# Kernel optimization log

Measured on AMD Instinct MI355X. Metric: run time of the kernel, lower is better.

## Reference

```python
import jax, jax.numpy as jnp
import numpy as np

N, G, E = 100000, 32768, 1000000
F, H = 64, 64


def _mlp(x, w1, b1, w2, b2):
    # Linear -> SiLU -> Linear (matches nn.Sequential in the torch module)
    return jax.nn.silu(x @ w1 + b1) @ w2 + b2


def setup_inputs() -> dict:
    key = jax.random.key(0)
    ks = jax.random.split(key, 24)

    def lin(k, fan_in, fan_out):
        s = 1.0 / np.sqrt(fan_in)
        kw, kb = jax.random.split(k)
        w = jax.random.uniform(kw, (fan_in, fan_out), jnp.float32, -s, s)
        b = jax.random.uniform(kb, (fan_out,), jnp.float32, -s, s)
        return w, b

    node_w1, node_b1 = lin(ks[0], F, H)
    node_w2, node_b2 = lin(ks[1], H, H)
    edge_w1, edge_b1 = lin(ks[2], 6, H)
    edge_w2, edge_b2 = lin(ks[3], H, H)
    msg_w1, msg_b1 = lin(ks[4], 2 * H, H)
    msg_w2, msg_b2 = lin(ks[5], H, H)
    upd_w1, upd_b1 = lin(ks[6], H, H)
    upd_w2, upd_b2 = lin(ks[7], H, H)

    return {
        "node_features": jax.random.normal(ks[8], (N, F), jnp.float32),
        "node_pos": jax.random.normal(ks[9], (N, 3), jnp.float32),
        "grid_pos": jax.random.normal(ks[10], (G, 3), jnp.float32),
        "orientations": jax.random.normal(ks[11], (N, 3, 3), jnp.float32),
        "edge_index": jnp.stack([
            jax.random.randint(ks[12], (E,), 0, N),
            jax.random.randint(ks[13], (E,), 0, G),
        ]),
        "node_w1": node_w1, "node_b1": node_b1, "node_w2": node_w2, "node_b2": node_b2,
        "edge_w1": edge_w1, "edge_b1": edge_b1, "edge_w2": edge_w2, "edge_b2": edge_b2,
        "msg_w1": msg_w1, "msg_b1": msg_b1, "msg_w2": msg_w2, "msg_b2": msg_b2,
        "upd_w1": upd_w1, "upd_b1": upd_b1, "upd_w2": upd_w2, "upd_b2": upd_b2,
    }


def reference(node_features, node_pos, grid_pos, orientations, edge_index,
              node_w1, node_b1, node_w2, node_b2,
              edge_w1, edge_b1, edge_w2, edge_b2,
              msg_w1, msg_b1, msg_w2, msg_b2,
              upd_w1, upd_b1, upd_w2, upd_b2):
    source, target = edge_index[0], edge_index[1]
    num_grid = grid_pos.shape[0]

    # node MLP
    h_node = _mlp(node_features, node_w1, node_b1, node_w2, node_b2)  # [N,H]

    # per-edge message with orientation-aware projection
    pos_s = node_pos[source]                 # [E,3]
    rel = grid_pos[target] - pos_s           # [E,3]
    # bmm(rel[:,None,:], R[source]).squeeze(1) == einsum ei,eij->ej
    trel = jnp.einsum("ei,eij->ej", rel, orientations[source])
    edge_attr = jnp.concatenate([pos_s, trel], axis=-1)        # [E,6]
    e_feat = _mlp(edge_attr, edge_w1, edge_b1, edge_w2, edge_b2)
    msg_in = jnp.concatenate([h_node[source], e_feat], axis=-1)  # [E,2H]
    messages = _mlp(msg_in, msg_w1, msg_b1, msg_w2, msg_b2)      # [E,H]

    # scatter-mean into grid buckets (mask out-of-range targets)
    valid = (target >= 0) & (target < num_grid)
    idx = jnp.where(valid, target, 0)
    msg_masked = jnp.where(valid[:, None], messages, 0.0)
    sums = jax.ops.segment_sum(msg_masked, idx, num_segments=num_grid)
    cnts = jax.ops.segment_sum(valid.astype(jnp.float32), idx, num_segments=num_grid)
    grid_feat = sums / jnp.maximum(cnts, 1.0)[:, None]

    return _mlp(grid_feat, upd_w1, upd_b1, upd_w2, upd_b2)  # [G,H]
```

## Files before the change

kernel.cpp:

```cpp
#include <hip/hip_runtime.h>
#include <hip/hip_bf16.h>
#include <cstdint>

typedef __attribute__((ext_vector_type(8))) short short8;
typedef __attribute__((ext_vector_type(4))) float f32x4;
typedef unsigned short u16;

__device__ __forceinline__ float b2f(u16 u) {
  union { unsigned int i; float f; } v; v.i = ((unsigned int)u) << 16; return v.f;
}
__device__ __forceinline__ u16 f2b(float f) {
  __hip_bfloat16 h = __float2bfloat16(f);
  union { __hip_bfloat16 h; u16 u; } v; v.h = h; return v.u;
}
__device__ __forceinline__ float silu_f(float x) { return x / (1.0f + __expf(-x)); }

__device__ __forceinline__ float loadF(const void* p, long i, int isf32) {
  if (isf32) return ((const float*)p)[i];
  return b2f(((const u16*)p)[i]);
}

__device__ __forceinline__ int sniffbit(u16 u) {
  unsigned e = (u >> 7) & 0xffu;
  return (e >= 0xC0u || (e < 0x40u && (u & 0x7fffu) != 0)) ? 1 : 0;
}
__device__ __forceinline__ int detect1(const void* p, int n) {
  const u16* q = (const u16*)p;
  int m = n < 512 ? n : 512;
  int h = 0;
  for (int k = 0; k < m; ++k) h += sniffbit(q[k]);
  return h >= 2;
}

struct Ptrs { const void* p[20]; };

#define FW_EW1 0
#define FW_UW1 384
#define FW_UW2 4480
#define FW_UB1 8576
#define FW_UB2 8640
#define FW_EB1 8704
#define FW_EB2 8768
#define FW_MB1 8832
#define FW_MB2 8896
#define FW_TOTAL 8960

#define IMG_EW2 0
#define IMG_MW1 4608
#define IMG_MW2 13312
#define IMG_TOTAL 17920

#define PREP_BLOCKS 105
#define HIST_BLOCKS 1024

__global__ __launch_bounds__(256) void fused_a(
    Ptrs a, u16* __restrict__ img, float* __restrict__ fw,
    const int* __restrict__ eidx, int* __restrict__ cnt,
    const void* x, u16* __restrict__ hout, int nrows,
    long E, int G, int nodeBlocks)
{
  const int t = threadIdx.x;
  const int b = blockIdx.x;

  if (b >= nodeBlocks + PREP_BLOCKS) {
    long i = (long)(b - nodeBlocks - PREP_BLOCKS) * 256 + t;
    const long stride = (long)HIST_BLOCKS * 256;
    for (; i < E; i += stride) {
      int tg = eidx[E + i];
      if (tg >= 0 && tg < G) atomicAdd(&cnt[tg], 1);
    }
    return;
  }

  if (b >= nodeBlocks) {
    int i = (b - nodeBlocks) * 256 + t;
    if (i < IMG_TOTAL) {
      const void* bp; int n; long si; bool real;
      if (i < IMG_MW1) { int nn = i / 72, k = i % 72; bp = a.p[10]; n = 4096; real = k < 64; si = (long)k * 64 + nn; }
      else if (i < IMG_MW2) { int t2 = i - IMG_MW1; int nn = t2 / 136, k = t2 % 136; bp = a.p[12]; n = 8192; real = k < 128; si = (long)k * 64 + nn; }
      else { int t2 = i - IMG_MW2; int nn = t2 / 72, k = t2 % 72; bp = a.p[14]; n = 4096; real = k < 64; si = (long)k * 64 + nn; }
      u16 val = 0;
      if (real) { int isf = detect1(bp, n); val = f2b(loadF(bp, si, isf)); }
      img[i] = val;
    } else if (i < IMG_TOTAL + FW_TOTAL) {
      int j = i - IMG_TOTAL;
      const void* bp; int n; long si;
      if (j < 384)        { bp = a.p[8];  n = 384;  si = j; }
      else if (j < 4480)  { bp = a.p[16]; n = 4096; si = j - 384; }
      else if (j < 8576)  { bp = a.p[18]; n = 4096; si = j - 4480; }
      else {
        int bb = j - 8576; int seg = bb >> 6; si = bb & 63; n = 64;
        switch (seg) {
          case 0: bp = a.p[17]; break;
          case 1: bp = a.p[19]; break;
          case 2: bp = a.p[9];  break;
          case 3: bp = a.p[11]; break;
          case 4: bp = a.p[13]; break;
          default: bp = a.p[15]; break;
        }
      }
      int isf = detect1(bp, n);
      fw[j] = loadF(bp, si, isf);
    }
    return;
  }

  __shared__ float xs[64][68];
  __shared__ float w1s[64][68];
  __shared__ float w2s[64][68];
  __shared__ float b1s[64];
  __shared__ float b2s[64];
  __shared__ int nd[5];
  if (t < 5) nd[t] = 0;
  __syncthreads();
  {
    int c = 0;
    const u16* q0 = (const u16*)x;
    for (int i = t; i < 2048; i += 256) c += sniffbit(q0[i]);
    if (c) atomicAdd(&nd[0], c);
    c = 0;
    const u16* q1 = (const u16*)a.p[4];
    for (int i = t; i < 2048; i += 256) c += sniffbit(q1[i]);
    if (c) atomicAdd(&nd[1], c);
    c = 0;
    const u16* q2 = (const u16*)a.p[6];
    for (int i = t; i < 2048; i += 256) c += sniffbit(q2[i]);
    if (c) atomicAdd(&nd[2], c);
    if (t < 64) {
      if (sniffbit(((const u16*)a.p[5])[t])) atomicAdd(&nd[3], 1);
      if (sniffbit(((const u16*)a.p[7])[t])) atomicAdd(&nd[4], 1);
    }
  }
  __syncthreads();
  const int xf = nd[0] >= 2, f1 = nd[1] >= 2, f2 = nd[2] >= 2;
  const int fb1 = nd[3] >= 2, fb2 = nd[4] >= 2;
  const long rbase = (long)b * 64;
  for (int i = t; i < 4096; i += 256) {
    int k = i >> 6, cc = i & 63;
    w1s[k][cc] = loadF(a.p[4], i, f1);
    w2s[k][cc] = loadF(a.p[6], i, f2);
  }
  if (t < 64) { b1s[t] = loadF(a.p[5], t, fb1); b2s[t] = loadF(a.p[7], t, fb2); }
  {
    int row = t >> 2, ch = t & 3;
    long rg = rbase + row;
    if (rg < nrows) {
      if (xf) {
        const float* xp = (const float*)x + rg * 64 + ch * 16;
#pragma unroll
        for (int m = 0; m < 16; ++m) xs[row][ch * 16 + m] = xp[m];
      } else {
        const u16* xp = (const u16*)x + rg * 64 + ch * 16;
#pragma unroll
        for (int m = 0; m < 16; ++m) xs[row][ch * 16 + m] = b2f(xp[m]);
      }
    } else {
#pragma unroll
      for (int m = 0; m < 16; ++m) xs[row][ch * 16 + m] = 0.f;
    }
  }
  __syncthreads();
  const int r0 = (t >> 4) * 4, c0 = (t & 15) * 4;
  float acc[4][4];
#pragma unroll
  for (int i = 0; i < 4; ++i)
#pragma unroll
    for (int j = 0; j < 4; ++j) acc[i][j] = b1s[c0 + j];
  for (int k = 0; k < 64; ++k) {
    float w0 = w1s[k][c0], w1v = w1s[k][c0 + 1], w2v = w1s[k][c0 + 2], w3v = w1s[k][c0 + 3];
#pragma unroll
    for (int i = 0; i < 4; ++i) {
      float av = xs[r0 + i][k];
      acc[i][0] = fmaf(av, w0, acc[i][0]);
      acc[i][1] = fmaf(av, w1v, acc[i][1]);
      acc[i][2] = fmaf(av, w2v, acc[i][2]);
      acc[i][3] = fmaf(av, w3v, acc[i][3]);
    }
  }
  __syncthreads();
#pragma unroll
  for (int i = 0; i < 4; ++i)
#pragma unroll
    for (int j = 0; j < 4; ++j) xs[r0 + i][c0 + j] = silu_f(acc[i][j]);
  __syncthreads();
  float acc2[4][4];
#pragma unroll
  for (int i = 0; i < 4; ++i)
#pragma unroll
    for (int j = 0; j < 4; ++j) acc2[i][j] = b2s[c0 + j];
  for (int k = 0; k < 64; ++k) {
    float w0 = w2s[k][c0], w1v = w2s[k][c0 + 1], w2v = w2s[k][c0 + 2], w3v = w2s[k][c0 + 3];
#pragma unroll
    for (int i = 0; i < 4; ++i) {
      float av = xs[r0 + i][k];
      acc2[i][0] = fmaf(av, w0, acc2[i][0]);
      acc2[i][1] = fmaf(av, w1v, acc2[i][1]);
      acc2[i][2] = fmaf(av, w2v, acc2[i][2]);
      acc2[i][3] = fmaf(av, w3v, acc2[i][3]);
    }
  }
#pragma unroll
  for (int i = 0; i < 4; ++i) {
    long rg = rbase + r0 + i;
    if (rg < nrows) {
#pragma unroll
      for (int j = 0; j < 4; ++j) hout[rg * 64 + c0 + j] = f2b(acc2[i][j]);
    }
  }
}

__global__ __launch_bounds__(256) void scan_k(const int* __restrict__ cnt,
                                              int* __restrict__ cursor,
                                              int* __restrict__ bsum, int G) {
  __shared__ int sd[256];
  const int t = threadIdx.x;
  int i = blockIdx.x * 256 + t;
  int v = (i < G) ? cnt[i] : 0;
  sd[t] = v;
  __syncthreads();
  for (int off = 1; off < 256; off <<= 1) {
    int x2 = (t >= off) ? sd[t - off] : 0;
    __syncthreads();
    sd[t] += x2;
    __syncthreads();
  }
  if (i < G) cursor[i] = sd[t] - v;
  if (t == 255) bsum[blockIdx.x] = sd[255];
}

__global__ __launch_bounds__(256) void scat_k(const int* __restrict__ eidx,
                                              int* __restrict__ cursor,
                                              const int* __restrict__ bsum,
                                              unsigned int* __restrict__ pkS,
                                              int* __restrict__ evp,
                                              long E, int G, int NB2) {
  __shared__ int bo[256];
  const int t = threadIdx.x;
  int v = (t < NB2) ? bsum[t] : 0;
  bo[t] = v;
  __syncthreads();
  for (int off = 1; off < 256; off <<= 1) {
    int x2 = (t >= off) ? bo[t - off] : 0;
    __syncthreads();
    bo[t] += x2;
    __syncthreads();
  }
  if (blockIdx.x == 0 && t == 0) *evp = bo[NB2 - 1];
  int excl = bo[t] - v;
  __syncthreads();
  bo[t] = excl;
  __syncthreads();
  long i = (long)blockIdx.x * 256 + t;
  const long stride = (long)gridDim.x * 256;
  for (; i < E; i += stride) {
    int tg = eidx[E + i];
    if (tg >= 0 && tg < G) {
      int s = eidx[i];
      int p = atomicAdd(&cursor[tg], 1) + bo[tg >> 8];
      pkS[p] = (unsigned int)s | ((unsigned int)tg << 17);
    }
  }
}

#define ETILES 4

__global__ __launch_bounds__(256, 5) void edge_kernel(
    const void* node_pos, const void* grid_pos, const void* orient,
    const unsigned int* __restrict__ pkS, const int* __restrict__ evp,
    const u16* __restrict__ h_node, const u16* __restrict__ img,
    const float* __restrict__ fw,
    float* __restrict__ sums, int G)
{
  __shared__ __align__(16) u16 hA[64][136];
  __shared__ __align__(16) u16 ef1[64][72];
  __shared__ float eaf[64][6];
  __shared__ float w1e[6][64];
  __shared__ float biasE[4][64];
  __shared__ int src_s[64];
  __shared__ int tgt_s[64];
  __shared__ int det[3];
  float (*msgf)[66] = (float (*)[66])&hA[0][0];

  const int t = threadIdx.x;
  if (t < 3) det[t] = 0;
  __syncthreads();
  {
    int grp = t >> 6;
    if (grp < 3) {
      const u16* qq = (const u16*)(grp == 0 ? node_pos : grp == 1 ? grid_pos : orient);
      int cth = 0, l = t & 63;
      for (int i = l; i < 2048; i += 64) cth += sniffbit(qq[i]);
      if (cth) atomicAdd(&det[grp], cth);
    }
  }
  for (int i = t; i < 384; i += 256) w1e[i / 64][i % 64] = fw[FW_EW1 + i];
  { int seg = t >> 6, cc = t & 63; biasE[seg][cc] = fw[FW_EB1 + seg * 64 + cc]; }
  __syncthreads();
  const int pf = det[0] >= 2, gf = det[1] >= 2, of = det[2] >= 2;
  const int Ev = *evp;

  const int lane = t & 63, w = t >> 6;
  const int q = lane >> 4, c = lane & 15;
  const int m0 = w * 16;
  const u16* wE2 = img + IMG_EW2;
  const u16* wM1 = img + IMG_MW1;
  const u16* wM2 = img + IMG_MW2;
  const f32x4 z = {0.f, 0.f, 0.f, 0.f};

  for (int tile = 0; tile < ETILES; ++tile) {
    long base = ((long)blockIdx.x * ETILES + tile) * 64;
    if (base >= Ev) break;
    __syncthreads();
    if (t < 64) {
      long eg = base + t;
      int s, tg;
      if (eg < Ev) {
        unsigned int pk = pkS[eg];
        s = (int)(pk & 0x1FFFFu);
        tg = (int)(pk >> 17);
      } else { s = 0; tg = -1; }
      src_s[t] = s;
      tgt_s[t] = tg;
      int tgc = (tg >= 0) ? tg : 0;
      float ps[3], rel[3], tr[3];
#pragma unroll
      for (int i = 0; i < 3; ++i) {
        ps[i] = loadF(node_pos, (long)s * 3 + i, pf);
        rel[i] = loadF(grid_pos, (long)tgc * 3 + i, gf) - ps[i];
      }
#pragma unroll
      for (int j = 0; j < 3; ++j) tr[j] = 0.f;
#pragma unroll
      for (int i = 0; i < 3; ++i)
#pragma unroll
        for (int j = 0; j < 3; ++j)
          tr[j] = fmaf(rel[i], loadF(orient, (long)s * 9 + i * 3 + j, of), tr[j]);
      eaf[t][0] = ps[0]; eaf[t][1] = ps[1]; eaf[t][2] = ps[2];
      eaf[t][3] = tr[0]; eaf[t][4] = tr[1]; eaf[t][5] = tr[2];
    }
    __syncthreads();
    {
      int e = t >> 2, ch = t & 3;
      const u16* hp = h_node + (long)src_s[e] * 64 + ch * 16;
      short8 v0 = *(const short8*)hp;
      short8 v1 = *(const short8*)(hp + 8);
      *(short8*)&hA[e][ch * 16] = v0;
      *(short8*)&hA[e][ch * 16 + 8] = v1;
    }
    __syncthreads();

    {
      int e = t >> 2, c0 = (t & 3) * 16;
      float a0 = eaf[e][0], a1 = eaf[e][1], a2 = eaf[e][2];
      float a3 = eaf[e][3], a4 = eaf[e][4], a5 = eaf[e][5];
      __align__(16) u16 tmp[16];
#pragma unroll
      for (int j = 0; j < 16; ++j) {
        int cc = c0 + j;
        float acc = biasE[0][cc];
        acc = fmaf(a0, w1e[0][cc], acc);
        acc = fmaf(a1, w1e[1][cc], acc);
        acc = fmaf(a2, w1e[2][cc], acc);
        acc = fmaf(a3, w1e[3][cc], acc);
        acc = fmaf(a4, w1e[4][cc], acc);
        acc = fmaf(a5, w1e[5][cc], acc);
        tmp[j] = f2b(silu_f(acc));
      }
      *(short8*)&ef1[e][c0] = *(const short8*)tmp;
      *(short8*)&ef1[e][c0 + 8] = *(const short8*)(tmp + 8);
    }
    __syncthreads();
    {
      short8 a0 = *(const short8*)&ef1[m0 + c][q * 8];
      short8 a1 = *(const short8*)&ef1[m0 + c][32 + q * 8];
#pragma unroll
      for (int nt = 0; nt < 4; ++nt) {
        short8 b0 = *(const short8*)&wE2[(nt * 16 + c) * 72 + q * 8];
        short8 b1v = *(const short8*)&wE2[(nt * 16 + c) * 72 + 32 + q * 8];
        f32x4 acc = __builtin_amdgcn_mfma_f32_16x16x32_bf16(a0, b0, z, 0, 0, 0);
        acc = __builtin_amdgcn_mfma_f32_16x16x32_bf16(a1, b1v, acc, 0, 0, 0);
#pragma unroll
        for (int r = 0; r < 4; ++r) {
          int row = m0 + q * 4 + r, col = nt * 16 + c;
          hA[row][64 + col] = f2b(acc[r] + biasE[1][col]);
        }
      }
    }
    __syncthreads();
    {
      short8 a0 = *(const short8*)&hA[m0 + c][q * 8];
      short8 a1 = *(const short8*)&hA[m0 + c][32 + q * 8];
      short8 a2 = *(const short8*)&hA[m0 + c][64 + q * 8];
      short8 a3 = *(const short8*)&hA[m0 + c][96 + q * 8];
#pragma unroll
      for (int nt = 0; nt < 4; ++nt) {
        const u16* wp = &wM1[(nt * 16 + c) * 136];
        f32x4 acc = __builtin_amdgcn_mfma_f32_16x16x32_bf16(a0, *(const short8*)(wp + q * 8), z, 0, 0, 0);
        acc = __builtin_amdgcn_mfma_f32_16x16x32_bf16(a1, *(const short8*)(wp + 32 + q * 8), acc, 0, 0, 0);
        acc = __builtin_amdgcn_mfma_f32_16x16x32_bf16(a2, *(const short8*)(wp + 64 + q * 8), acc, 0, 0, 0);
        acc = __builtin_amdgcn_mfma_f32_16x16x32_bf16(a3, *(const short8*)(wp + 96 + q * 8), acc, 0, 0, 0);
#pragma unroll
        for (int r = 0; r < 4; ++r) {
          int row = m0 + q * 4 + r, col = nt * 16 + c;
          ef1[row][col] = f2b(silu_f(acc[r] + biasE[2][col]));
        }
      }
    }
    __syncthreads();
    {
      short8 a0 = *(const short8*)&ef1[m0 + c][q * 8];
      short8 a1 = *(const short8*)&ef1[m0 + c][32 + q * 8];
#pragma unroll
      for (int nt = 0; nt < 4; ++nt) {
        short8 b0 = *(const short8*)&wM2[(nt * 16 + c) * 72 + q * 8];
        short8 b1v = *(const short8*)&wM2[(nt * 16 + c) * 72 + 32 + q * 8];
        f32x4 acc = __builtin_amdgcn_mfma_f32_16x16x32_bf16(a0, b0, z, 0, 0, 0);
        acc = __builtin_amdgcn_mfma_f32_16x16x32_bf16(a1, b1v, acc, 0, 0, 0);
#pragma unroll
        for (int r = 0; r < 4; ++r) {
          int row = m0 + q * 4 + r, col = nt * 16 + c;
          msgf[row][col] = acc[r] + biasE[3][col];
        }
      }
    }
    __syncthreads();
    {
      int col = lane;
      int r0 = w * 16;
      int cur = tgt_s[r0];
      float run = msgf[r0][col];
      bool lopen = (r0 == 0) ? true : (tgt_s[r0 - 1] == cur);
#pragma unroll
      for (int r2 = 1; r2 < 16; ++r2) {
        int r = r0 + r2;
        int tg = tgt_s[r];
        float v = msgf[r][col];
        if (tg == cur) {
          run += v;
        } else {
          if (cur >= 0) {
            if (lopen) unsafeAtomicAdd(&sums[(long)cur * 64 + col], run);
            else sums[(long)cur * 64 + col] = run;
          }
          cur = tg; run = v; lopen = false;
        }
      }
      bool ropen = (r0 + 16 >= 64) ? true : (tgt_s[r0 + 16] == cur);
      if (cur >= 0) {
        if (lopen || ropen) unsafeAtomicAdd(&sums[(long)cur * 64 + col], run);
        else sums[(long)cur * 64 + col] = run;
      }
    }
  }
}

__global__ __launch_bounds__(256) void upd_mlp(
    const float* __restrict__ sums, const int* __restrict__ cnt,
    const float* __restrict__ fw, float* __restrict__ out, int nrows)
{
  __shared__ float xs[64][68];
  __shared__ float w1s[64][68];
  __shared__ float w2s[64][68];
  __shared__ float b1s[64];
  __shared__ float b2s[64];
  const int t = threadIdx.x;
  const long rbase = (long)blockIdx.x * 64;
  for (int i = t; i < 4096; i += 256) {
    int k = i >> 6, cc = i & 63;
    w1s[k][cc] = fw[FW_UW1 + i];
    w2s[k][cc] = fw[FW_UW2 + i];
  }
  if (t < 64) { b1s[t] = fw[FW_UB1 + t]; b2s[t] = fw[FW_UB2 + t]; }
  {
    int row = t >> 2, ch = t & 3;
    long rg = rbase + row;
    if (rg < nrows) {
      float inv = 1.0f / fmaxf((float)cnt[rg], 1.0f);
      const float* p = sums + rg * 64 + ch * 16;
#pragma unroll
      for (int m = 0; m < 16; ++m) xs[row][ch * 16 + m] = p[m] * inv;
    } else {
#pragma unroll
      for (int m = 0; m < 16; ++m) xs[row][ch * 16 + m] = 0.f;
    }
  }
  __syncthreads();
  const int r0 = (t >> 4) * 4, c0 = (t & 15) * 4;
  float acc[4][4];
#pragma unroll
  for (int i = 0; i < 4; ++i)
#pragma unroll
    for (int j = 0; j < 4; ++j) acc[i][j] = b1s[c0 + j];
  for (int k = 0; k < 64; ++k) {
    float w0 = w1s[k][c0], w1v = w1s[k][c0 + 1], w2v = w1s[k][c0 + 2], w3v = w1s[k][c0 + 3];
#pragma unroll
    for (int i = 0; i < 4; ++i) {
      float av = xs[r0 + i][k];
      acc[i][0] = fmaf(av, w0, acc[i][0]);
      acc[i][1] = fmaf(av, w1v, acc[i][1]);
      acc[i][2] = fmaf(av, w2v, acc[i][2]);
      acc[i][3] = fmaf(av, w3v, acc[i][3]);
    }
  }
  __syncthreads();
#pragma unroll
  for (int i = 0; i < 4; ++i)
#pragma unroll
    for (int j = 0; j < 4; ++j) xs[r0 + i][c0 + j] = silu_f(acc[i][j]);
  __syncthreads();
  float acc2[4][4];
#pragma unroll
  for (int i = 0; i < 4; ++i)
#pragma unroll
    for (int j = 0; j < 4; ++j) acc2[i][j] = b2s[c0 + j];
  for (int k = 0; k < 64; ++k) {
    float w0 = w2s[k][c0], w1v = w2s[k][c0 + 1], w2v = w2s[k][c0 + 2], w3v = w2s[k][c0 + 3];
#pragma unroll
    for (int i = 0; i < 4; ++i) {
      float av = xs[r0 + i][k];
      acc2[i][0] = fmaf(av, w0, acc2[i][0]);
      acc2[i][1] = fmaf(av, w1v, acc2[i][1]);
      acc2[i][2] = fmaf(av, w2v, acc2[i][2]);
      acc2[i][3] = fmaf(av, w3v, acc2[i][3]);
    }
  }
#pragma unroll
  for (int i = 0; i < 4; ++i) {
    long rg = rbase + r0 + i;
    if (rg < nrows) {
#pragma unroll
      for (int j = 0; j < 4; ++j) out[rg * 64 + c0 + j] = acc2[i][j];
    }
  }
}

extern "C" void kernel_launch(void* const* d_in, const int* in_sizes, int n_in,
                              void* d_out, int out_size, void* d_ws, size_t ws_size,
                              hipStream_t stream) {
  const int N = in_sizes[1] / 3;
  const int G = in_sizes[2] / 3;
  const long E = (long)in_sizes[4] / 2;
  const int NB2 = (G + 255) / 256;
  const int nodeBlocks = (N + 63) / 64;

  char* ws = (char*)d_ws;
  float* sums = (float*)ws;
  size_t off = (size_t)G * 256;
  int* cnt = (int*)(ws + off);     off += (size_t)G * 4;
  int* cursor = (int*)(ws + off);  off += (size_t)G * 4;
  int* bsum = (int*)(ws + off);    off += 1024;
  int* evp = (int*)(ws + off);     off += 256;
  unsigned int* pkS = (unsigned int*)(ws + off); off += (size_t)E * 4;
  u16* h_node = (u16*)(ws + off);  off += (size_t)N * 128;
  u16* img = (u16*)(ws + off);     off += (size_t)IMG_TOTAL * 2;
  float* fw = (float*)(ws + off);

  hipMemsetAsync(ws, 0, (size_t)G * 260, stream);

  Ptrs a;
  const int map[20] = {0,1,2,3, 5,6,7,8, 9,10,11,12, 13,14,15,16, 17,18,19,20};
  for (int i = 0; i < 20; ++i) a.p[i] = d_in[map[i]];

  fused_a<<<nodeBlocks + PREP_BLOCKS + HIST_BLOCKS, 256, 0, stream>>>(
      a, img, fw, (const int*)d_in[4], cnt, d_in[0], h_node, N, E, G, nodeBlocks);
  scan_k<<<NB2, 256, 0, stream>>>(cnt, cursor, bsum, G);
  scat_k<<<1024, 256, 0, stream>>>((const int*)d_in[4], cursor, bsum, pkS, evp, E, G, NB2);
  edge_kernel<<<(int)((E + ETILES * 64 - 1) / (ETILES * 64)), 256, 0, stream>>>(
      d_in[1], d_in[2], d_in[3], pkS, evp, h_node, img, fw, sums, G);
  upd_mlp<<<(G + 63) / 64, 256, 0, stream>>>(sums, cnt, fw, (float*)d_out, G);
}
```

Measured before the change: 488.0 us.

## Hoist dtype detection into a dedicated kernel and enlarge edge tiles per block

Adds a tiny detect_k kernel that computes a per-input fp32/bf16 flag once and stores it in workspace. fused_a and edge_kernel now read these flags instead of re-sniffing thousands of elements in every block, and detect1 no longer runs per element in the prep blocks. Other changes: edge tiles per block go from 4 to 8, the src shared array is replaced by re-reading pkS, a per-tile barrier moves, and the packed scatter store becomes nontemporal. The cost is one extra kernel launch and a dependency on the flags buffer.

After: 474.4 us. -2.8%, faster.

```diff
diff --git a/kernel.cpp b/kernel.cpp
--- a/kernel.cpp
+++ b/kernel.cpp
@@ -24,15 +24,8 @@
   unsigned e = (u >> 7) & 0xffu;
   return (e >= 0xC0u || (e < 0x40u && (u & 0x7fffu) != 0)) ? 1 : 0;
 }
-__device__ __forceinline__ int detect1(const void* p, int n) {
-  const u16* q = (const u16*)p;
-  int m = n < 512 ? n : 512;
-  int h = 0;
-  for (int k = 0; k < m; ++k) h += sniffbit(q[k]);
-  return h >= 2;
-}
-
-struct Ptrs { const void* p[20]; };
+
+struct Ptrs { const void* p[20]; int n[20]; };
 
 #define FW_EW1 0
 #define FW_UW1 384
@@ -53,17 +46,32 @@
 #define PREP_BLOCKS 105
 #define HIST_BLOCKS 1024
 
+__global__ __launch_bounds__(256) void detect_k(Ptrs a, int* flags) {
+  int j = blockIdx.x;
+  const u16* q = (const u16*)a.p[j];
+  int n = a.n[j];
+  int m = n < 4096 ? n : 4096;
+  int cnt = 0;
+  for (int i = threadIdx.x; i < m; i += 256) cnt += sniffbit(q[i]);
+  __shared__ int tot;
+  if (threadIdx.x == 0) tot = 0;
+  __syncthreads();
+  if (cnt) atomicAdd(&tot, cnt);
+  __syncthreads();
+  if (threadIdx.x == 0) flags[j] = (tot >= 2) ? 1 : 0;
+}
+
 __global__ __launch_bounds__(256) void fused_a(
-    Ptrs a, u16* __restrict__ img, float* __restrict__ fw,
+    Ptrs a, const int* __restrict__ flags,
+    u16* __restrict__ img, float* __restrict__ fw,
     const int* __restrict__ eidx, int* __restrict__ cnt,
-    const void* x, u16* __restrict__ hout, int nrows,
-    long E, int G, int nodeBlocks)
+    u16* __restrict__ hout, int nrows, long E, int G)
 {
   const int t = threadIdx.x;
   const int b = blockIdx.x;
 
-  if (b >= nodeBlocks + PREP_BLOCKS) {
-    long i = (long)(b - nodeBlocks - PREP_BLOCKS) * 256 + t;
+  if (b < HIST_BLOCKS) {
+    long i = (long)b * 256 + t;
     const long stride = (long)HIST_BLOCKS * 256;
     for (; i < E; i += stride) {
       int tg = eidx[E + i];
@@ -72,35 +80,34 @@
     return;
   }
 
-  if (b >= nodeBlocks) {
-    int i = (b - nodeBlocks) * 256 + t;
+  if (b < HIST_BLOCKS + PREP_BLOCKS) {
+    int i = (b - HIST_BLOCKS) * 256 + t;
     if (i < IMG_TOTAL) {
-      const void* bp; int n; long si; bool real;
-      if (i < IMG_MW1) { int nn = i / 72, k = i % 72; bp = a.p[10]; n = 4096; real = k < 64; si = (long)k * 64 + nn; }
-      else if (i < IMG_MW2) { int t2 = i - IMG_MW1; int nn = t2 / 136, k = t2 % 136; bp = a.p[12]; n = 8192; real = k < 128; si = (long)k * 64 + nn; }
-      else { int t2 = i - IMG_MW2; int nn = t2 / 72, k = t2 % 72; bp = a.p[14]; n = 4096; real = k < 64; si = (long)k * 64 + nn; }
+      const void* bp; int fl; long si; bool real;
+      if (i < IMG_MW1) { int nn = i / 72, k = i % 72; bp = a.p[10]; fl = flags[10]; real = k < 64; si = (long)k * 64 + nn; }
+      else if (i < IMG_MW2) { int t2 = i - IMG_MW1; int nn = t2 / 136, k = t2 % 136; bp = a.p[12]; fl = flags[12]; real = k < 128; si = (long)k * 64 + nn; }
+      else { int t2 = i - IMG_MW2; int nn = t2 / 72, k = t2 % 72; bp = a.p[14]; fl = flags[14]; real = k < 64; si = (long)k * 64 + nn; }
       u16 val = 0;
-      if (real) { int isf = detect1(bp, n); val = f2b(loadF(bp, si, isf)); }
+      if (real) val = f2b(loadF(bp, si, fl));
       img[i] = val;
     } else if (i < IMG_TOTAL + FW_TOTAL) {
       int j = i - IMG_TOTAL;
-      const void* bp; int n; long si;
-      if (j < 384)        { bp = a.p[8];  n = 384;  si = j; }
-      else if (j < 4480)  { bp = a.p[16]; n = 4096; si = j - 384; }
-      else if (j < 8576)  { bp = a.p[18]; n = 4096; si = j - 4480; }
+      const void* bp; int fl; long si;
+      if (j < 384)        { bp = a.p[8];  fl = flags[8];  si = j; }
+      else if (j < 4480)  { bp = a.p[16]; fl = flags[16]; si = j - 384; }
+      else if (j < 8576)  { bp = a.p[18]; fl = flags[18]; si = j - 4480; }
       else {
-        int bb = j - 8576; int seg = bb >> 6; si = bb & 63; n = 64;
+        int bb = j - 8576; int seg = bb >> 6; si = bb & 63;
         switch (seg) {
-          case 0: bp = a.p[17]; break;
-          case 1: bp = a.p[19]; break;
-          case 2: bp = a.p[9];  break;
-          case 3: bp = a.p[11]; break;
-          case 4: bp = a.p[13]; break;
-          default: bp = a.p[15]; break;
+          case 0: bp = a.p[17]; fl = flags[17]; break;
+          case 1: bp = a.p[19]; fl = flags[19]; break;
+          case 2: bp = a.p[9];  fl = flags[9];  break;
+          case 3: bp = a.p[11]; fl = flags[11]; break;
+          case 4: bp = a.p[13]; fl = flags[13]; break;
+          default: bp = a.p[15]; fl = flags[15]; break;
         }
       }
-      int isf = detect1(bp, n);
-      fw[j] = loadF(bp, si, isf);
+      fw[j] = loadF(bp, si, fl);
     }
     return;
   }
@@ -110,31 +117,9 @@
   __shared__ float w2s[64][68];
   __shared__ float b1s[64];
   __shared__ float b2s[64];
-  __shared__ int nd[5];
-  if (t < 5) nd[t] = 0;
-  __syncthreads();
-  {
-    int c = 0;
-    const u16* q0 = (const u16*)x;
-    for (int i = t; i < 2048; i += 256) c += sniffbit(q0[i]);
-    if (c) atomicAdd(&nd[0], c);
-    c = 0;
-    const u16* q1 = (const u16*)a.p[4];
-    for (int i = t; i < 2048; i += 256) c += sniffbit(q1[i]);
-    if (c) atomicAdd(&nd[1], c);
-    c = 0;
-    const u16* q2 = (const u16*)a.p[6];
-    for (int i = t; i < 2048; i += 256) c += sniffbit(q2[i]);
-    if (c) atomicAdd(&nd[2], c);
-    if (t < 64) {
-      if (sniffbit(((const u16*)a.p[5])[t])) atomicAdd(&nd[3], 1);
-      if (sniffbit(((const u16*)a.p[7])[t])) atomicAdd(&nd[4], 1);
-    }
-  }
-  __syncthreads();
-  const int xf = nd[0] >= 2, f1 = nd[1] >= 2, f2 = nd[2] >= 2;
-  const int fb1 = nd[3] >= 2, fb2 = nd[4] >= 2;
-  const long rbase = (long)b * 64;
+  const void* x = a.p[0];
+  const int xf = flags[0], f1 = flags[4], fb1 = flags[5], f2 = flags[6], fb2 = flags[7];
+  const long rbase = (long)(b - HIST_BLOCKS - PREP_BLOCKS) * 64;
   for (int i = t; i < 4096; i += 256) {
     int k = i >> 6, cc = i & 63;
     w1s[k][cc] = loadF(a.p[4], i, f1);
@@ -257,18 +242,18 @@
     if (tg >= 0 && tg < G) {
       int s = eidx[i];
       int p = atomicAdd(&cursor[tg], 1) + bo[tg >> 8];
-      pkS[p] = (unsigned int)s | ((unsigned int)tg << 17);
-    }
-  }
-}
-
-#define ETILES 4
+      __builtin_nontemporal_store((unsigned int)s | ((unsigned int)tg << 17), pkS + p);
+    }
+  }
+}
+
+#define ETILES 8
 
 __global__ __launch_bounds__(256, 5) void edge_kernel(
     const void* node_pos, const void* grid_pos, const void* orient,
     const unsigned int* __restrict__ pkS, const int* __restrict__ evp,
     const u16* __restrict__ h_node, const u16* __restrict__ img,
-    const float* __restrict__ fw,
+    const float* __restrict__ fw, const int* __restrict__ flags,
     float* __restrict__ sums, int G)
 {
   __shared__ __align__(16) u16 hA[64][136];
@@ -276,28 +261,15 @@
   __shared__ float eaf[64][6];
   __shared__ float w1e[6][64];
   __shared__ float biasE[4][64];
-  __shared__ int src_s[64];
   __shared__ int tgt_s[64];
-  __shared__ int det[3];
   float (*msgf)[66] = (float (*)[66])&hA[0][0];
 
   const int t = threadIdx.x;
-  if (t < 3) det[t] = 0;
-  __syncthreads();
-  {
-    int grp = t >> 6;
-    if (grp < 3) {
-      const u16* qq = (const u16*)(grp == 0 ? node_pos : grp == 1 ? grid_pos : orient);
-      int cth = 0, l = t & 63;
-      for (int i = l; i < 2048; i += 64) cth += sniffbit(qq[i]);
-      if (cth) atomicAdd(&det[grp], cth);
-    }
-  }
+  const int pf = flags[1], gf = flags[2], of = flags[3];
+  const int Ev = *evp;
   for (int i = t; i < 384; i += 256) w1e[i / 64][i % 64] = fw[FW_EW1 + i];
   { int seg = t >> 6, cc = t & 63; biasE[seg][cc] = fw[FW_EB1 + seg * 64 + cc]; }
   __syncthreads();
-  const int pf = det[0] >= 2, gf = det[1] >= 2, of = det[2] >= 2;
-  const int Ev = *evp;
 
   const int lane = t & 63, w = t >> 6;
   const int q = lane >> 4, c = lane & 15;
@@ -310,16 +282,14 @@
   for (int tile = 0; tile < ETILES; ++tile) {
     long base = ((long)blockIdx.x * ETILES + tile) * 64;
     if (base >= Ev) break;
-    __syncthreads();
     if (t < 64) {
       long eg = base + t;
-      int s, tg;
+      int s = 0, tg = -1;
       if (eg < Ev) {
         unsigned int pk = pkS[eg];
         s = (int)(pk & 0x1FFFFu);
         tg = (int)(pk >> 17);
-      } else { s = 0; tg = -1; }
-      src_s[t] = s;
+      }
       tgt_s[t] = tg;
       int tgc = (tg >= 0) ? tg : 0;
       float ps[3], rel[3], tr[3];
@@ -338,10 +308,12 @@
       eaf[t][0] = ps[0]; eaf[t][1] = ps[1]; eaf[t][2] = ps[2];
       eaf[t][3] = tr[0]; eaf[t][4] = tr[1]; eaf[t][5] = tr[2];
     }
-    __syncthreads();
     {
       int e = t >> 2, ch = t & 3;
-      const u16* hp = h_node + (long)src_s[e] * 64 + ch * 16;
+      long eg = base + e;
+      int s = 0;
+      if (eg < Ev) s = (int)(pkS[eg] & 0x1FFFFu);
+      const u16* hp = h_node + (long)s * 64 + ch * 16;
       short8 v0 = *(const short8*)hp;
       short8 v1 = *(const short8*)(hp + 8);
       *(short8*)&hA[e][ch * 16] = v0;
@@ -451,6 +423,7 @@
         else sums[(long)cur * 64 + col] = run;
       }
     }
+    __syncthreads();
   }
 }
 
@@ -550,6 +523,7 @@
   int* cursor = (int*)(ws + off);  off += (size_t)G * 4;
   int* bsum = (int*)(ws + off);    off += 1024;
   int* evp = (int*)(ws + off);     off += 256;
+  int* flags = (int*)(ws + off);   off += 256;
   unsigned int* pkS = (unsigned int*)(ws + off); off += (size_t)E * 4;
   u16* h_node = (u16*)(ws + off);  off += (size_t)N * 128;
   u16* img = (u16*)(ws + off);     off += (size_t)IMG_TOTAL * 2;
@@ -559,13 +533,14 @@
 
   Ptrs a;
   const int map[20] = {0,1,2,3, 5,6,7,8, 9,10,11,12, 13,14,15,16, 17,18,19,20};
-  for (int i = 0; i < 20; ++i) a.p[i] = d_in[map[i]];
-
-  fused_a<<<nodeBlocks + PREP_BLOCKS + HIST_BLOCKS, 256, 0, stream>>>(
-      a, img, fw, (const int*)d_in[4], cnt, d_in[0], h_node, N, E, G, nodeBlocks);
+  for (int i = 0; i < 20; ++i) { a.p[i] = d_in[map[i]]; a.n[i] = in_sizes[map[i]]; }
+
+  detect_k<<<20, 256, 0, stream>>>(a, flags);
+  fused_a<<<HIST_BLOCKS + PREP_BLOCKS + nodeBlocks, 256, 0, stream>>>(
+      a, flags, img, fw, (const int*)d_in[4], cnt, h_node, N, E, G);
   scan_k<<<NB2, 256, 0, stream>>>(cnt, cursor, bsum, G);
   scat_k<<<1024, 256, 0, stream>>>((const int*)d_in[4], cursor, bsum, pkS, evp, E, G, NB2);
   edge_kernel<<<(int)((E + ETILES * 64 - 1) / (ETILES * 64)), 256, 0, stream>>>(
-      d_in[1], d_in[2], d_in[3], pkS, evp, h_node, img, fw, sums, G);
+      d_in[1], d_in[2], d_in[3], pkS, evp, h_node, img, fw, flags, sums, G);
   upd_mlp<<<(G + 63) / 64, 256, 0, stream>>>(sums, cnt, fw, (float*)d_out, G);
 }
```
